# Kernel tuning notes

Measured on AMD Instinct MI355X. Metric: run time of the kernel, lower is better.

## Reference

```python
import jax, jax.numpy as jnp
import numpy as np

B, N, C = 2, 2048, 1024
H = 16
D = C // H  # head_dim = 64
SCALE = D ** -0.5


def setup_inputs() -> dict:
    key = jax.random.key(0)
    ks = jax.random.split(key, 9)
    s = C ** -0.5  # ~ torch Linear default init scale
    return {
        "x": jax.random.normal(ks[0], (B, N, C), dtype=jnp.float32),
        "Wq": jax.random.uniform(ks[1], (C, C), jnp.float32, -s, s),
        "bq": jax.random.uniform(ks[2], (C,), jnp.float32, -s, s),
        "Wk": jax.random.uniform(ks[3], (C, C), jnp.float32, -s, s),
        "bk": jax.random.uniform(ks[4], (C,), jnp.float32, -s, s),
        "Wv": jax.random.uniform(ks[5], (C, C), jnp.float32, -s, s),
        "bv": jax.random.uniform(ks[6], (C,), jnp.float32, -s, s),
        "Wo": jax.random.uniform(ks[7], (C, C), jnp.float32, -s, s),
        "bo": jax.random.uniform(ks[8], (C,), jnp.float32, -s, s),
    }


def reference(x, Wq, bq, Wk, bk, Wv, bv, Wo, bo):
    # Projections: [B,N,C] -> [B,H,N,D]
    def split_heads(t):
        return t.reshape(B, N, H, D).transpose(0, 2, 1, 3)

    q = split_heads(x @ Wq.T + bq)
    k = split_heads(x @ Wk.T + bk)
    v = split_heads(x @ Wv.T + bv)

    scores = jnp.einsum("bhnd,bhmd->bhnm", q, k) * SCALE  # [B,H,N,N]
    attn = jax.nn.softmax(scores, axis=-1)
    out = jnp.einsum("bhnm,bhmd->bhnd", attn, v)  # [B,H,N,D]
    out = out.transpose(0, 2, 1, 3).reshape(B, N, C)
    return out @ Wo.T + bo
```

## Files before the change

### kernel.cpp

```cpp
#include <hip/hip_runtime.h>
#include <stdint.h>


typedef _Float16 h8 __attribute__((ext_vector_type(8)));
typedef _Float16 h4 __attribute__((ext_vector_type(4)));
typedef float f4 __attribute__((ext_vector_type(4)));
typedef float f16f __attribute__((ext_vector_type(16)));
typedef uint32_t u32;
typedef u32 u32x4 __attribute__((ext_vector_type(4)));

#define AS1(p) ((const __attribute__((address_space(1))) void*)(p))
#define AS3(p) ((__attribute__((address_space(3))) void*)(p))

template <int ITERS>
__device__ __forceinline__ void stage128B(const _Float16* g, int ldk, _Float16* s, int tid) {
#pragma unroll
  for (int j = 0; j < ITERS; ++j) {
    int off = j * 4096 + tid * 16;
    int row = off >> 7;
    int ch = (off >> 4) & 7;
    int gch = ch ^ (row & 7);
    __builtin_amdgcn_global_load_lds(AS1(g + row * ldk + gch * 8), AS3(s + (off >> 1)), 16, 0, 0);
  }
}

__device__ __forceinline__ void stage_vt(const _Float16* g, _Float16* s, int tid) {
#pragma unroll
  for (int j = 0; j < 4; ++j) {
    int off = j * 4096 + tid * 16;
    int row = off >> 8;
    int ch = (off >> 4) & 15;
    int gch = ch ^ (row & 15);
    __builtin_amdgcn_global_load_lds(AS1(g + row * 2048 + gch * 8), AS3(s + (off >> 1)), 16, 0, 0);
  }
}

__device__ __forceinline__ h8 frag64(const _Float16* s, int row, int g) {
  return *(const h8*)(s + row * 64 + ((g ^ (row & 7)) << 3));
}

__global__ void cvt_all(const float* __restrict__ x, const float* __restrict__ Wq,
                        const float* __restrict__ Wk, const float* __restrict__ Wv,
                        const float* __restrict__ Wo, _Float16* __restrict__ xh,
                        _Float16* __restrict__ q, _Float16* __restrict__ k,
                        _Float16* __restrict__ v, _Float16* __restrict__ o) {
  int blk = blockIdx.x;
  const float* src; _Float16* dst; int off;
  if (blk < 4096)      { src = x;  dst = xh; off = blk; }
  else if (blk < 5120) { src = Wq; dst = q;  off = blk - 4096; }
  else if (blk < 6144) { src = Wk; dst = k;  off = blk - 5120; }
  else if (blk < 7168) { src = Wv; dst = v;  off = blk - 6144; }
  else                 { src = Wo; dst = o;  off = blk - 7168; }
  int i = off * 1024 + threadIdx.x * 4;
  f4 vv = *(const f4*)(src + i);
  h4 ov;
  ov[0] = (_Float16)vv[0]; ov[1] = (_Float16)vv[1]; ov[2] = (_Float16)vv[2]; ov[3] = (_Float16)vv[3];
  *(h4*)(dst + i) = ov;
}

__global__ __launch_bounds__(256, 3) void gemm_qkv(
    const _Float16* __restrict__ X,
    const _Float16* __restrict__ W0, const _Float16* __restrict__ W1, const _Float16* __restrict__ W2,
    const float* __restrict__ b0, const float* __restrict__ b1, const float* __restrict__ b2,
    _Float16* __restrict__ O0, _Float16* __restrict__ O1, _Float16* __restrict__ O2) {
  __shared__ _Float16 As[128 * 64];
  __shared__ _Float16 Bs[128 * 64];
  int z = blockIdx.z;
  const _Float16* W = (z == 0) ? W0 : (z == 1) ? W1 : W2;
  const float* bias = (z == 0) ? b0 : (z == 1) ? b1 : b2;

  int tid = threadIdx.x;
  int lane = tid & 63, wave = tid >> 6;
  int quad = lane >> 4, l15 = lane & 15;
  int wm = (wave >> 1) << 6, wn = (wave & 1) << 6;
  int m0 = blockIdx.y << 7, n0 = blockIdx.x << 7;

  f4 acc[4][4] = {};
  for (int k0 = 0; k0 < 1024; k0 += 64) {
    stage128B<4>(X + m0 * 1024 + k0, 1024, As, tid);
    stage128B<4>(W + n0 * 1024 + k0, 1024, Bs, tid);
    __syncthreads();
#pragma unroll
    for (int ks = 0; ks < 2; ++ks) {
      h8 af[4], bf[4];
#pragma unroll
      for (int i = 0; i < 4; ++i) af[i] = frag64(As, wm + i * 16 + l15, ks * 4 + quad);
#pragma unroll
      for (int i = 0; i < 4; ++i) bf[i] = frag64(Bs, wn + i * 16 + l15, ks * 4 + quad);
#pragma unroll
      for (int mi = 0; mi < 4; ++mi)
#pragma unroll
        for (int ni = 0; ni < 4; ++ni)
          acc[mi][ni] = __builtin_amdgcn_mfma_f32_16x16x32_f16(af[mi], bf[ni], acc[mi][ni], 0, 0, 0);
    }
    __syncthreads();
  }

  if (z == 2) {
#pragma unroll
    for (int mi = 0; mi < 4; ++mi) {
#pragma unroll
      for (int ni = 0; ni < 4; ++ni) {
        int o = n0 + wn + ni * 16 + l15;
        float bv = bias[o];
        int h = o >> 6, dd = o & 63;
        int m = m0 + wm + mi * 16 + quad * 4;
        int b = m >> 11, n = m & 2047;
        h4 v;
#pragma unroll
        for (int r = 0; r < 4; ++r) v[r] = (_Float16)(acc[mi][ni][r] + bv);
        *(h4*)(O2 + (((b * 16 + h) * 64 + dd) * 2048 + n)) = v;
      }
    }
  } else {
    float scale = (z == 0) ? 0.125f * 1.44269504089f : 1.0f;
    _Float16* Out = (z == 0) ? O0 : O1;
#pragma unroll
    for (int mi = 0; mi < 4; ++mi) {
#pragma unroll
      for (int ni = 0; ni < 4; ++ni) {
        int o = n0 + wn + ni * 16 + l15;
        float bv = bias[o];
        int h = o >> 6, d = o & 63;
#pragma unroll
        for (int r = 0; r < 4; ++r) {
          int m = m0 + wm + mi * 16 + quad * 4 + r;
          int b = m >> 11, n = m & 2047;
          float v = (acc[mi][ni][r] + bv) * scale;
          Out[(((b * 16 + h) * 2048 + n) << 6) + d] = (_Float16)v;
        }
      }
    }
  }
}

__global__ __launch_bounds__(256, 3) void gemm_out(
    const _Float16* __restrict__ A, const _Float16* __restrict__ W,
    const float* __restrict__ bias, float* __restrict__ Out) {
  __shared__ _Float16 As[128 * 64];
  __shared__ _Float16 Bs[64 * 64];
  int tid = threadIdx.x;
  int lane = tid & 63, wave = tid >> 6;
  int quad = lane >> 4, l15 = lane & 15;
  int wm = (wave >> 1) << 6, wn = (wave & 1) << 5;
  int m0 = blockIdx.y << 7, n0 = blockIdx.x << 6;

  f4 acc[4][2] = {};
  for (int k0 = 0; k0 < 1024; k0 += 64) {
    stage128B<4>(A + m0 * 1024 + k0, 1024, As, tid);
    stage128B<2>(W + n0 * 1024 + k0, 1024, Bs, tid);
    __syncthreads();
#pragma unroll
    for (int ks = 0; ks < 2; ++ks) {
      h8 af[4], bf[2];
#pragma unroll
      for (int i = 0; i < 4; ++i) af[i] = frag64(As, wm + i * 16 + l15, ks * 4 + quad);
#pragma unroll
      for (int i = 0; i < 2; ++i) bf[i] = frag64(Bs, wn + i * 16 + l15, ks * 4 + quad);
#pragma unroll
      for (int mi = 0; mi < 4; ++mi)
#pragma unroll
        for (int ni = 0; ni < 2; ++ni)
          acc[mi][ni] = __builtin_amdgcn_mfma_f32_16x16x32_f16(af[mi], bf[ni], acc[mi][ni], 0, 0, 0);
    }
    __syncthreads();
  }
#pragma unroll
  for (int mi = 0; mi < 4; ++mi) {
#pragma unroll
    for (int ni = 0; ni < 2; ++ni) {
      int o = n0 + wn + ni * 16 + l15;
      float bv = bias[o];
#pragma unroll
      for (int r = 0; r < 4; ++r) {
        int m = m0 + wm + mi * 16 + quad * 4 + r;
        Out[m * 1024 + o] = acc[mi][ni][r] + bv;
      }
    }
  }
}

__global__ __launch_bounds__(256, 2) void attn(
    const _Float16* __restrict__ Q, const _Float16* __restrict__ Kv,
    const _Float16* __restrict__ Vt, _Float16* __restrict__ AO) {
  __shared__ _Float16 Ks[2][128 * 64];
  __shared__ _Float16 Vs[2][64 * 128];
  int tid = threadIdx.x, lane = tid & 63, wave = tid >> 6;
  int h = lane >> 5, l31 = lane & 31;
  int bh = blockIdx.y, q0 = blockIdx.x << 7;

  const _Float16* Qb = Q + (bh * 2048 + q0 + wave * 32 + l31) * 64;
  h8 qf[4];
#pragma unroll
  for (int ks4 = 0; ks4 < 4; ++ks4)
    qf[ks4] = *(const h8*)(Qb + ks4 * 16 + h * 8);

  int krow = (l31 & 19) | ((l31 & 4) << 1) | ((l31 & 8) >> 1);
  int kch = krow & 7;
  int vch = l31 & 15;

  const _Float16* Kb = Kv + bh * 131072;
  const _Float16* Vb = Vt + bh * 131072;
  f16f oacc[2] = {};
  float lsum = 0.f;

  stage128B<4>(Kb, 64, Ks[0], tid);
  stage_vt(Vb, Vs[0], tid);

  for (int kt = 0; kt < 16; ++kt) {
    int cur = kt & 1;
    __syncthreads();
    if (kt < 15) {
      stage128B<4>(Kb + (kt + 1) * 8192, 64, Ks[cur ^ 1], tid);
      stage_vt(Vb + (kt + 1) * 128, Vs[cur ^ 1], tid);
    }
    const _Float16* Kst = Ks[cur];
    const _Float16* Vst = Vs[cur];

    f16f sacc[4] = {};
#pragma unroll
    for (int ks4 = 0; ks4 < 4; ++ks4) {
      int pch = ((ks4 * 2 + h) ^ kch) << 3;
#pragma unroll
      for (int kt2 = 0; kt2 < 4; ++kt2) {
        h8 kf = *(const h8*)(Kst + kt2 * 2048 + krow * 64 + pch);
        sacc[kt2] = __builtin_amdgcn_mfma_f32_32x32x16_f16(kf, qf[ks4], sacc[kt2], 0, 0, 0);
      }
    }

    u32 pkw[4][8];
#pragma unroll
    for (int g = 0; g < 4; ++g) {
#pragma unroll
      for (int i = 0; i < 8; ++i) {
        float pa = __builtin_amdgcn_exp2f(sacc[g][2 * i]);
        float pb = __builtin_amdgcn_exp2f(sacc[g][2 * i + 1]);
        lsum += pa + pb;
        pkw[g][i] = __builtin_bit_cast(u32, __builtin_amdgcn_cvt_pkrtz(pa, pb));
      }
    }

#pragma unroll
    for (int g = 0; g < 4; ++g) {
#pragma unroll
      for (int s = 0; s < 2; ++s) {
        u32x4 pw = {pkw[g][4 * s], pkw[g][4 * s + 1], pkw[g][4 * s + 2], pkw[g][4 * s + 3]};
        h8 pb = __builtin_bit_cast(h8, pw);
        int ch = ((g * 4 + s * 2 + h) ^ vch) << 3;
#pragma unroll
        for (int dt = 0; dt < 2; ++dt) {
          h8 vf = *(const h8*)(Vst + (dt * 32 + l31) * 128 + ch);
          oacc[dt] = __builtin_amdgcn_mfma_f32_32x32x16_f16(vf, pb, oacc[dt], 0, 0, 0);
        }
      }
    }
  }

  float l = lsum + __shfl_xor(lsum, 32);
  float inv = 1.0f / l;
  int b = bh >> 4, hh = bh & 15;
  int n = q0 + wave * 32 + l31;
  _Float16* base = AO + (b * 2048 + n) * 1024 + hh * 64;
#pragma unroll
  for (int dt = 0; dt < 2; ++dt) {
#pragma unroll
    for (int b2 = 0; b2 < 4; ++b2) {
      h4 o;
#pragma unroll
      for (int a = 0; a < 4; ++a) o[a] = (_Float16)(oacc[dt][b2 * 4 + a] * inv);
      *(h4*)(base + dt * 32 + b2 * 8 + h * 4) = o;
    }
  }
}

extern "C" void kernel_launch(void* const* d_in, const int* in_sizes, int n_in,
                              void* d_out, int out_size, void* d_ws, size_t ws_size,
                              hipStream_t stream) {
  const float* x = (const float*)d_in[0];
  const float* Wq = (const float*)d_in[1];
  const float* bq = (const float*)d_in[2];
  const float* Wk = (const float*)d_in[3];
  const float* bk = (const float*)d_in[4];
  const float* Wv = (const float*)d_in[5];
  const float* bv = (const float*)d_in[6];
  const float* Wo = (const float*)d_in[7];
  const float* bo = (const float*)d_in[8];
  float* out = (float*)d_out;

  char* w = (char*)d_ws;
  _Float16* xh  = (_Float16*)(w);
  _Float16* Wqh = (_Float16*)(w + (8u << 20));
  _Float16* Wkh = (_Float16*)(w + (10u << 20));
  _Float16* Wvh = (_Float16*)(w + (12u << 20));
  _Float16* Woh = (_Float16*)(w + (14u << 20));
  _Float16* Qh  = (_Float16*)(w + (16u << 20));
  _Float16* Kh  = (_Float16*)(w + (24u << 20));
  _Float16* Vth = (_Float16*)(w + (32u << 20));
  _Float16* AOh = xh;

  cvt_all<<<8192, 256, 0, stream>>>(x, Wq, Wk, Wv, Wo, xh, Wqh, Wkh, Wvh, Woh);
  gemm_qkv<<<dim3(8, 32, 3), 256, 0, stream>>>(xh, Wqh, Wkh, Wvh, bq, bk, bv, Qh, Kh, Vth);
  attn<<<dim3(16, 32), 256, 0, stream>>>(Qh, Kh, Vth, AOh);
  gemm_out<<<dim3(16, 32), 256, 0, stream>>>(AOh, Woh, bo, out);
}
```

Baseline: 179.7 us.

## Give each wave private K/V staging buffers and drop block-wide barriers

The attention kernel now splits the shared K/V tiles into per-wave double buffers of 32 keys. Each wave stages its own copy with global_load_lds and synchronises with s_waitcnt instead of __syncthreads. This removes block-level barrier stalls and lets waves run independently. In exchange every wave loads the same K/V data, so global/L2 traffic into LDS is four times larger, and each iteration does less work with more loop overhead (64 steps instead of 16). Relying only on vmcnt without a barrier also risks subtle ordering issues when LDS writes from global_load_lds complete.

```diff
diff --git a/kernel.cpp b/kernel.cpp
--- a/kernel.cpp
+++ b/kernel.cpp
@@ -24,14 +24,25 @@
   }
 }
 
-__device__ __forceinline__ void stage_vt(const _Float16* g, _Float16* s, int tid) {
+__device__ __forceinline__ void stage_k32(const _Float16* g, _Float16* s, int lane) {
 #pragma unroll
   for (int j = 0; j < 4; ++j) {
-    int off = j * 4096 + tid * 16;
-    int row = off >> 8;
-    int ch = (off >> 4) & 15;
-    int gch = ch ^ (row & 15);
-    __builtin_amdgcn_global_load_lds(AS1(g + row * 2048 + gch * 8), AS3(s + (off >> 1)), 16, 0, 0);
+    int off = j * 1024 + lane * 16;
+    int row = off >> 7;
+    int ch = (off >> 4) & 7;
+    __builtin_amdgcn_global_load_lds(AS1(g + row * 64 + ((ch ^ (row & 7)) << 3)),
+                                     AS3(s + (off >> 1)), 16, 0, 0);
+  }
+}
+
+__device__ __forceinline__ void stage_v32(const _Float16* g, _Float16* s, int lane) {
+#pragma unroll
+  for (int j = 0; j < 4; ++j) {
+    int off = j * 1024 + lane * 16;
+    int row = off >> 6;
+    int ch = (off >> 4) & 3;
+    __builtin_amdgcn_global_load_lds(AS1(g + row * 2048 + ((ch ^ (row & 3)) << 3)),
+                                     AS3(s + (off >> 1)), 16, 0, 0);
   }
 }
 
@@ -183,8 +194,8 @@
 __global__ __launch_bounds__(256, 2) void attn(
     const _Float16* __restrict__ Q, const _Float16* __restrict__ Kv,
     const _Float16* __restrict__ Vt, _Float16* __restrict__ AO) {
-  __shared__ _Float16 Ks[2][128 * 64];
-  __shared__ _Float16 Vs[2][64 * 128];
+  __shared__ _Float16 KsA[4][2][32 * 64];
+  __shared__ _Float16 VsA[4][2][64 * 32];
   int tid = threadIdx.x, lane = tid & 63, wave = tid >> 6;
   int h = lane >> 5, l31 = lane & 31;
   int bh = blockIdx.y, q0 = blockIdx.x << 7;
@@ -196,62 +207,57 @@
     qf[ks4] = *(const h8*)(Qb + ks4 * 16 + h * 8);
 
   int krow = (l31 & 19) | ((l31 & 4) << 1) | ((l31 & 8) >> 1);
-  int kch = krow & 7;
-  int vch = l31 & 15;
+  int kch7 = krow & 7;
+  int vch3 = l31 & 3;
 
   const _Float16* Kb = Kv + bh * 131072;
   const _Float16* Vb = Vt + bh * 131072;
+  _Float16* Ksw0 = &KsA[wave][0][0];
+  _Float16* Ksw1 = &KsA[wave][1][0];
+  _Float16* Vsw0 = &VsA[wave][0][0];
+  _Float16* Vsw1 = &VsA[wave][1][0];
+
   f16f oacc[2] = {};
   float lsum = 0.f;
 
-  stage128B<4>(Kb, 64, Ks[0], tid);
-  stage_vt(Vb, Vs[0], tid);
-
-  for (int kt = 0; kt < 16; ++kt) {
-    int cur = kt & 1;
-    __syncthreads();
-    if (kt < 15) {
-      stage128B<4>(Kb + (kt + 1) * 8192, 64, Ks[cur ^ 1], tid);
-      stage_vt(Vb + (kt + 1) * 128, Vs[cur ^ 1], tid);
-    }
-    const _Float16* Kst = Ks[cur];
-    const _Float16* Vst = Vs[cur];
-
-    f16f sacc[4] = {};
+  stage_k32(Kb, Ksw0, lane);
+  stage_v32(Vb, Vsw0, lane);
+
+  for (int t = 0; t < 64; ++t) {
+    const _Float16* Kst = (t & 1) ? Ksw1 : Ksw0;
+    const _Float16* Vst = (t & 1) ? Vsw1 : Vsw0;
+    if (t < 63) {
+      asm volatile("s_waitcnt lgkmcnt(0)" ::: "memory");
+      stage_k32(Kb + (t + 1) * 2048, (t & 1) ? Ksw0 : Ksw1, lane);
+      stage_v32(Vb + (t + 1) * 32, (t & 1) ? Vsw0 : Vsw1, lane);
+    }
+    asm volatile("s_waitcnt vmcnt(8)" ::: "memory");
+
+    f16f sacc = {};
 #pragma unroll
     for (int ks4 = 0; ks4 < 4; ++ks4) {
-      int pch = ((ks4 * 2 + h) ^ kch) << 3;
-#pragma unroll
-      for (int kt2 = 0; kt2 < 4; ++kt2) {
-        h8 kf = *(const h8*)(Kst + kt2 * 2048 + krow * 64 + pch);
-        sacc[kt2] = __builtin_amdgcn_mfma_f32_32x32x16_f16(kf, qf[ks4], sacc[kt2], 0, 0, 0);
-      }
-    }
-
-    u32 pkw[4][8];
-#pragma unroll
-    for (int g = 0; g < 4; ++g) {
-#pragma unroll
-      for (int i = 0; i < 8; ++i) {
-        float pa = __builtin_amdgcn_exp2f(sacc[g][2 * i]);
-        float pb = __builtin_amdgcn_exp2f(sacc[g][2 * i + 1]);
-        lsum += pa + pb;
-        pkw[g][i] = __builtin_bit_cast(u32, __builtin_amdgcn_cvt_pkrtz(pa, pb));
-      }
-    }
-
-#pragma unroll
-    for (int g = 0; g < 4; ++g) {
-#pragma unroll
-      for (int s = 0; s < 2; ++s) {
-        u32x4 pw = {pkw[g][4 * s], pkw[g][4 * s + 1], pkw[g][4 * s + 2], pkw[g][4 * s + 3]};
-        h8 pb = __builtin_bit_cast(h8, pw);
-        int ch = ((g * 4 + s * 2 + h) ^ vch) << 3;
-#pragma unroll
-        for (int dt = 0; dt < 2; ++dt) {
-          h8 vf = *(const h8*)(Vst + (dt * 32 + l31) * 128 + ch);
-          oacc[dt] = __builtin_amdgcn_mfma_f32_32x32x16_f16(vf, pb, oacc[dt], 0, 0, 0);
-        }
+      h8 kf = *(const h8*)(Kst + krow * 64 + (((ks4 * 2 + h) ^ kch7) << 3));
+      sacc = __builtin_amdgcn_mfma_f32_32x32x16_f16(kf, qf[ks4], sacc, 0, 0, 0);
+    }
+
+    u32 pkw[8];
+#pragma unroll
+    for (int i = 0; i < 8; ++i) {
+      float pa = __builtin_amdgcn_exp2f(sacc[2 * i]);
+      float pb = __builtin_amdgcn_exp2f(sacc[2 * i + 1]);
+      lsum += pa + pb;
+      pkw[i] = __builtin_bit_cast(u32, __builtin_amdgcn_cvt_pkrtz(pa, pb));
+    }
+
+#pragma unroll
+    for (int s = 0; s < 2; ++s) {
+      u32x4 pw = {pkw[4 * s], pkw[4 * s + 1], pkw[4 * s + 2], pkw[4 * s + 3]};
+      h8 pb = __builtin_bit_cast(h8, pw);
+#pragma unroll
+      for (int dt = 0; dt < 2; ++dt) {
+        int row = dt * 32 + l31;
+        h8 vf = *(const h8*)(Vst + row * 32 + (((s * 2 + h) ^ vch3) << 3));
+        oacc[dt] = __builtin_amdgcn_mfma_f32_32x32x16_f16(vf, pb, oacc[dt], 0, 0, 0);
       }
     }
   }
```

Result: slower. 186.7 us (+3.9%).
